# Performance work log

Measured on AMD Instinct MI355X. Metric: run time of the kernel, lower is better.

Reference implementation:

```python
import jax, jax.numpy as jnp
import numpy as np

B, S, D = 4, 2048, 1024
NH, NKV = 16, 4
HD = D // NH  # 64


def _rope(x, freqs):
    # x: [B, H, S, HD], freqs: [B, S, HD//2]
    cos = jnp.concatenate([jnp.cos(freqs), jnp.cos(freqs)], axis=-1)[:, None]  # [B,1,S,HD]
    sin = jnp.concatenate([jnp.sin(freqs), jnp.sin(freqs)], axis=-1)[:, None]
    x1, x2 = x[..., : HD // 2], x[..., HD // 2:]
    rot = jnp.concatenate([-x2, x1], axis=-1)
    return x * cos + rot * sin


def setup_inputs() -> dict:
    key = jax.random.key(0)
    ks = jax.random.split(key, 9)
    return {
        "hidden_states": jax.random.normal(ks[0], (B, S, D), jnp.float32),
        "rotary_pos_emb": jax.random.normal(ks[1], (B, S, HD // 2), jnp.float32),
        "Wq": jax.random.normal(ks[2], (D, NH * HD), jnp.float32) * 0.02,
        "bq": jax.random.normal(ks[3], (NH * HD,), jnp.float32) * 0.02,
        "Wk": jax.random.normal(ks[4], (D, NKV * HD), jnp.float32) * 0.02,
        "bk": jax.random.normal(ks[5], (NKV * HD,), jnp.float32) * 0.02,
        "Wv": jax.random.normal(ks[6], (D, NKV * HD), jnp.float32) * 0.02,
        "bv": jax.random.normal(ks[7], (NKV * HD,), jnp.float32) * 0.02,
        "Wo": jax.random.normal(ks[8], (NH * HD, D), jnp.float32) * 0.02,
    }


def reference(hidden_states, rotary_pos_emb, Wq, bq, Wk, bk, Wv, bv, Wo):
    b, s, _ = hidden_states.shape
    # projections -> [B, H, S, HD]
    q = (hidden_states @ Wq + bq).reshape(b, s, NH, HD).transpose(0, 2, 1, 3)
    k = (hidden_states @ Wk + bk).reshape(b, s, NKV, HD).transpose(0, 2, 1, 3)
    v = (hidden_states @ Wv + bv).reshape(b, s, NKV, HD).transpose(0, 2, 1, 3)
    q = _rope(q, rotary_pos_emb)
    k = _rope(k, rotary_pos_emb)
    groups = NH // NKV
    k = jnp.repeat(k, groups, axis=1)  # [B, NH, S, HD]
    v = jnp.repeat(v, groups, axis=1)
    scaling = HD ** -0.5
    scores = jnp.einsum("bhqd,bhkd->bhqk", q, k) * scaling
    probs = jax.nn.softmax(scores.astype(jnp.float32), axis=-1).astype(q.dtype)
    out = jnp.einsum("bhqk,bhkd->bhqd", probs, v)
    out = out.transpose(0, 2, 1, 3).reshape(b, s, NH * HD)
    return out @ Wo
```

## Files before the change

### kernel.cpp

```cpp
#include <hip/hip_runtime.h>
#include <hip/hip_bf16.h>

#define BB 4
#define SS 2048
#define DD 1024
#define NH 16
#define NKV 4
#define HD 64
#define MROWS (BB*SS)
#define NQKV (NH*HD + 2*NKV*HD)
#define KOFF (NH*HD)

typedef short v8s __attribute__((ext_vector_type(8)));
typedef short v4s __attribute__((ext_vector_type(4)));
typedef float v4f __attribute__((ext_vector_type(4)));
typedef unsigned short u16;
typedef unsigned int u32;

__device__ __forceinline__ float bf2f(u16 u){
  union { float f; u32 i; } x; x.i = ((u32)u) << 16; return x.f;
}
__device__ __forceinline__ u16 f2bf(float f){
  union { __hip_bfloat16 h; u16 u; } x; x.h = __float2bfloat16(f); return x.u;
}
__device__ __forceinline__ u32 cvtpk(float lo, float hi){
  u32 r;
  asm("v_cvt_pk_bf16_f32 %0, %1, %2" : "=v"(r) : "v"(lo), "v"(hi));
  return r;
}
__device__ __forceinline__ void gl_lds16(const u16* g, u16* l){
  __builtin_amdgcn_global_load_lds(
      (const __attribute__((address_space(1))) u32*)g,
      (__attribute__((address_space(3))) u32*)l, 16, 0, 0);
}


__global__ void prep_fused(const float* __restrict__ Wq, const float* __restrict__ Wk,
                           const float* __restrict__ Wv, const float* __restrict__ bq,
                           const float* __restrict__ bk, const float* __restrict__ bv,
                           const float* __restrict__ Wo, const float* __restrict__ fr,
                           u16* __restrict__ Bqkv, float* __restrict__ bias,
                           u16* __restrict__ WoT, float2* __restrict__ trig){
  __shared__ float T[32][33];
  const int bid = blockIdx.x;
  const int tid = threadIdx.x;
  const int tx = tid & 31, ty = tid >> 5;
  if (bid < 1536) {
    const int kt = (bid & 31)*32, nt = (bid >> 5)*32;
    const int n = nt + tx;
    const float* src; int ld, nb;
    if (nt < 1024)      { src = Wq; ld = 1024; nb = n; }
    else if (nt < 1280) { src = Wk; ld = 256;  nb = n - 1024; }
    else                { src = Wv; ld = 256;  nb = n - 1280; }
    #pragma unroll
    for (int i=0;i<4;i++)
      T[ty + 8*i][tx] = src[(long)(kt + ty + 8*i)*ld + nb];
    __syncthreads();
    #pragma unroll
    for (int i=0;i<4;i++)
      Bqkv[(long)(nt + ty + 8*i)*1024 + kt + tx] = f2bf(T[tx][ty + 8*i]);
    if ((bid & 31) == 0 && ty == 0)
      bias[n] = (n < 1024) ? bq[n] : (n < 1280 ? bk[n-1024] : bv[n-1280]);
  } else if (bid < 2560) {
    const int b2 = bid - 1536;
    const int kt = (b2 & 31)*32, nt = (b2 >> 5)*32;
    #pragma unroll
    for (int i=0;i<4;i++)
      T[ty + 8*i][tx] = Wo[(long)(kt + ty + 8*i)*1024 + nt + tx];
    __syncthreads();
    #pragma unroll
    for (int i=0;i<4;i++)
      WoT[(long)(nt + ty + 8*i)*1024 + kt + tx] = f2bf(T[tx][ty + 8*i]);
  } else {
    int i = (bid - 2560)*256 + tid;
    float f = fr[i];
    float sn, cs; __sincosf(f, &sn, &cs);
    trig[i] = make_float2(cs, sn);
  }
}

__global__ void rope_k(u16* __restrict__ QKV, const float2* __restrict__ trig){
  int idx = blockIdx.x*256 + threadIdx.x;
  int d  = idx & 31;
  int hh = (idx >> 5) & 3;
  long row = idx >> 7;
  int col = KOFF + hh*HD + d;
  u16* p = QKV + row*NQKV;
  float x1 = bf2f(p[col]);
  float x2 = bf2f(p[col+32]);
  float2 t = trig[row*32 + d];
  p[col]    = f2bf(x1*t.x - x2*t.y);
  p[col+32] = f2bf(x2*t.x + x1*t.y);
}


template<bool BIAS, typename IT, typename OT>
__global__ __launch_bounds__(256) void gemm_bt(
    const IT* __restrict__ A, const u16* __restrict__ Bt,
    const float* __restrict__ bias, OT* __restrict__ C,
    int K, int ldc)
{
  __shared__ u16 As[128*32];
  __shared__ u16 Bs[128*32];
  const int tid = threadIdx.x;
  const int wid = tid >> 6, lane = tid & 63;
  const int g = lane >> 4, c = lane & 15;
  const long brow = (long)blockIdx.y * 128;
  const long bcol = (long)blockIdx.x * 128;
  const int wr = (wid >> 1) * 64, wc = (wid & 1) * 64;
  const int srow = tid >> 2;
  const int scol = (tid & 3) * 8;
  const IT*  ga = &A [(brow + srow)*K + scol];
  const u16* gb = &Bt[(bcol + srow)*K + scol];
  u16* la  = &As[(wid*64)*8];
  u16* lb  = &Bs[(wid*64)*8];
  u16* lwa = &As[srow*32 + scol];
  v4f acc[4][4] = {};
  for (int kt = 0; kt < K; kt += 32) {
    __syncthreads();
    gl_lds16(gb + kt,        lb);
    gl_lds16(gb + 64*K + kt, lb + 256*8);
    if constexpr (sizeof(IT) == 4) {
      float4 a0 = *reinterpret_cast<const float4*>(ga + kt);
      float4 a1 = *reinterpret_cast<const float4*>(ga + kt + 4);
      float4 a2 = *reinterpret_cast<const float4*>(ga + (long)64*K + kt);
      float4 a3 = *reinterpret_cast<const float4*>(ga + (long)64*K + kt + 4);
      union { v8s v; u32 w[4]; } p0, p1;
      p0.w[0] = cvtpk(a0.x, a0.y); p0.w[1] = cvtpk(a0.z, a0.w);
      p0.w[2] = cvtpk(a1.x, a1.y); p0.w[3] = cvtpk(a1.z, a1.w);
      p1.w[0] = cvtpk(a2.x, a2.y); p1.w[1] = cvtpk(a2.z, a2.w);
      p1.w[2] = cvtpk(a3.x, a3.y); p1.w[3] = cvtpk(a3.z, a3.w);
      *reinterpret_cast<v8s*>(lwa)          = p0.v;
      *reinterpret_cast<v8s*>(lwa + 64*32)  = p1.v;
    } else {
      gl_lds16((const u16*)ga + kt,        la);
      gl_lds16((const u16*)ga + 64*K + kt, la + 256*8);
    }
    __syncthreads();
    v8s af[4], bf[4];
    #pragma unroll
    for (int m=0;m<4;m++) af[m] = *reinterpret_cast<const v8s*>(&As[(wr + m*16 + c)*32 + g*8]);
    #pragma unroll
    for (int n=0;n<4;n++) bf[n] = *reinterpret_cast<const v8s*>(&Bs[(wc + n*16 + c)*32 + g*8]);
    __builtin_amdgcn_s_setprio(1);
    #pragma unroll
    for (int m=0;m<4;m++)
      #pragma unroll
      for (int n=0;n<4;n++)
        acc[m][n] = __builtin_amdgcn_mfma_f32_16x16x32_bf16(af[m], bf[n], acc[m][n], 0,0,0);
    __builtin_amdgcn_s_setprio(0);
  }
  #pragma unroll
  for (int m=0;m<4;m++)
    #pragma unroll
    for (int n=0;n<4;n++) {
      int col = (int)bcol + wc + n*16 + c;
      float badd = BIAS ? bias[col] : 0.0f;
      #pragma unroll
      for (int r2=0;r2<4;r2++){
        long row = brow + wr + m*16 + g*4 + r2;
        float v = acc[m][n][r2] + badd;
        if constexpr (sizeof(OT)==2) C[row*ldc + col] = (OT)f2bf(v);
        else                         C[row*ldc + col] = (OT)v;
      }
    }
}


__global__ __launch_bounds__(512) void attn_k(const u16* __restrict__ QKV,
                                              const float2* __restrict__ trig,
                                              u16* __restrict__ Out){
  __shared__ u16 Ks[4][64][72];
  __shared__ u16 Vs[4][64][72];
  const int tid = threadIdx.x;
  const int wid = tid >> 6, lane = tid & 63;
  const int g = lane >> 4, c = lane & 15;
  const int qt = blockIdx.x & 7;
  const int bh = blockIdx.x >> 3;
  const int b = bh >> 4, h = bh & 15;
  const int kvh = h >> 2;
  const u16* Qb = QKV + (long)b*SS*NQKV + h*HD;
  const u16* Kb = QKV + (long)b*SS*NQKV + KOFF + kvh*HD;
  const u16* Vb = Kb + NKV*HD;

  const float SCL = 0.125f * 1.44269504088896f;
  v8s qf[2][2];
  #pragma unroll
  for (int qn=0;qn<2;qn++){
    int lrow = qt*256 + wid*32 + qn*16 + c;
    v8s q0 = *reinterpret_cast<const v8s*>(&Qb[(long)lrow*NQKV + g*8]);
    v8s q1 = *reinterpret_cast<const v8s*>(&Qb[(long)lrow*NQKV + 32 + g*8]);
    const float2* tp = trig + ((long)b*SS + lrow)*32 + g*8;
    union { v8s v; u32 w[4]; } a0, a1;
    #pragma unroll
    for (int wi=0;wi<4;wi++){
      float2 ta = tp[2*wi], tb = tp[2*wi+1];
      float x1a = bf2f((u16)q0[2*wi]),   x2a = bf2f((u16)q1[2*wi]);
      float x1b = bf2f((u16)q0[2*wi+1]), x2b = bf2f((u16)q1[2*wi+1]);
      float r0a = (x1a*ta.x - x2a*ta.y) * SCL;
      float r1a = (x2a*ta.x + x1a*ta.y) * SCL;
      float r0b = (x1b*tb.x - x2b*tb.y) * SCL;
      float r1b = (x2b*tb.x + x1b*tb.y) * SCL;
      a0.w[wi] = cvtpk(r0a, r0b);
      a1.w[wi] = cvtpk(r1a, r1b);
    }
    qf[qn][0] = a0.v; qf[qn][1] = a1.v;
  }

  v8s onesf;
  {
    short ov = (c==0) ? (short)0x3F80 : (short)0;
    #pragma unroll
    for (int j=0;j<8;j++) onesf[j] = ov;
  }

  const v4f vzero = {0.f, 0.f, 0.f, 0.f};
  v4f o[2][5] = {};

  const int krow = tid >> 3;
  const int kcol = (tid & 7) * 8;
  const int key0 = 2*(tid >> 4);
  const int dg4  = (tid & 15) * 4;
  const int slot0 = 32*(key0>>5) + 8*((key0>>2)&3) + 4*((key0>>4)&1) + (key0&3);
  int vofs[4];
  #pragma unroll
  for (int j=0;j<4;j++){
    int d = dg4 + j;
    int idx = (((slot0>>3) ^ (d>>3)) << 3) | (slot0 & 7);
    vofs[j] = d*72 + idx;
  }
  u16* VsF = &Vs[0][0][0];

  const u16* kp  = Kb + (long)krow*NQKV + kcol;
  const u16* vp0 = Vb + (long)key0*NQKV + dg4;
  const u16* vp1 = vp0 + NQKV;

  v8s kregA, kregB;
  union { v4s v; u32 w[2]; } vrA0, vrA1, vrB0, vrB1;

  auto write_tile = [&](int q, const v8s& kr,
                        const u32* wA, const u32* wB){
    *reinterpret_cast<v8s*>(&Ks[q][krow][kcol]) = kr;
    const int bofs = q * (64*72);
    #pragma unroll
    for (int j=0;j<4;j++){
      u32 pkd = __builtin_amdgcn_perm(wB[j>>1], wA[j>>1],
                                      (j&1) ? 0x07060302u : 0x05040100u);
      *reinterpret_cast<u32*>(&VsF[bofs + vofs[j]]) = pkd;
    }
  };

  auto qk_tile = [&](int buf, v4f st[4][2]){
    v8s kf0[4], kf1[4];
    #pragma unroll
    for (int km=0;km<4;km++){
      kf0[km] = *reinterpret_cast<const v8s*>(&Ks[buf][km*16 + c][g*8]);
      kf1[km] = *reinterpret_cast<const v8s*>(&Ks[buf][km*16 + c][32 + g*8]);
    }
    __builtin_amdgcn_s_setprio(1);
    #pragma unroll
    for (int km=0;km<4;km++)
      #pragma unroll
      for (int qn=0;qn<2;qn++)
        st[km][qn] = __builtin_amdgcn_mfma_f32_16x16x32_bf16(kf0[km], qf[qn][0], vzero, 0,0,0);
    #pragma unroll
    for (int km=0;km<4;km++)
      #pragma unroll
      for (int qn=0;qn<2;qn++)
        st[km][qn] = __builtin_amdgcn_mfma_f32_16x16x32_bf16(kf1[km], qf[qn][1], st[km][qn], 0,0,0);
    __builtin_amdgcn_s_setprio(0);
  };
  auto exp_pack = [&](v4f st[4][2], v8s pa[2][2]){
    #pragma unroll
    for (int km=0;km<4;km++)
      #pragma unroll
      for (int qn=0;qn<2;qn++)
        #pragma unroll
        for (int r2=0;r2<4;r2++)
          st[km][qn][r2] = __builtin_amdgcn_exp2f(st[km][qn][r2]);
    #pragma unroll
    for (int qm=0;qm<2;qm++)
      #pragma unroll
      for (int ks=0;ks<2;ks++){
        union { v8s v; u32 w[4]; } u;
        u.w[0] = cvtpk(st[2*ks  ][qm][0], st[2*ks  ][qm][1]);
        u.w[1] = cvtpk(st[2*ks  ][qm][2], st[2*ks  ][qm][3]);
        u.w[2] = cvtpk(st[2*ks+1][qm][0], st[2*ks+1][qm][1]);
        u.w[3] = cvtpk(st[2*ks+1][qm][2], st[2*ks+1][qm][3]);
        pa[qm][ks] = u.v;
      }
  };
  auto pv_tile = [&](int buf, v8s pa[2][2]){
    #pragma unroll
    for (int ks=0;ks<2;ks++){
      __builtin_amdgcn_s_setprio(1);
      #pragma unroll
      for (int dn=0;dn<4;dn++){
        int d0 = dn*16 + c;
        v8s vf = *reinterpret_cast<const v8s*>(&Vs[buf][d0][(((ks*4+g) ^ (d0>>3)) << 3)]);
        #pragma unroll
        for (int qm=0;qm<2;qm++)
          o[qm][dn] = __builtin_amdgcn_mfma_f32_16x16x32_bf16(pa[qm][ks], vf, o[qm][dn], 0,0,0);
      }
      #pragma unroll
      for (int qm=0;qm<2;qm++)
        o[qm][4] = __builtin_amdgcn_mfma_f32_16x16x32_bf16(pa[qm][ks], onesf, o[qm][4], 0,0,0);
      __builtin_amdgcn_s_setprio(0);
    }
  };

  {
    long off1 = (long)64*NQKV;
    kregA  = *reinterpret_cast<const v8s*>(kp);
    vrA0.v = *reinterpret_cast<const v4s*>(vp0);
    vrA1.v = *reinterpret_cast<const v4s*>(vp1);
    kregB  = *reinterpret_cast<const v8s*>(kp  + off1);
    vrB0.v = *reinterpret_cast<const v4s*>(vp0 + off1);
    vrB1.v = *reinterpret_cast<const v4s*>(vp1 + off1);
    write_tile(0, kregA, vrA0.w, vrA1.w);
    write_tile(1, kregB, vrB0.w, vrB1.w);
  }
  __syncthreads();

  for (int j = 0; j < SS/128; ++j){
    const int base = (j & 1) * 2;
    const bool pf = (j + 1 < SS/128);
    if (pf) {
      long offA = (long)(2*j+2)*64*NQKV;
      long offB = (long)(2*j+3)*64*NQKV;
      kregA  = *reinterpret_cast<const v8s*>(kp  + offA);
      vrA0.v = *reinterpret_cast<const v4s*>(vp0 + offA);
      vrA1.v = *reinterpret_cast<const v4s*>(vp1 + offA);
      kregB  = *reinterpret_cast<const v8s*>(kp  + offB);
      vrB0.v = *reinterpret_cast<const v4s*>(vp0 + offB);
      vrB1.v = *reinterpret_cast<const v4s*>(vp1 + offB);
    }

    v4f stA[4][2];
    v8s paA[2][2], paB[2][2];
    qk_tile(base, stA);
    exp_pack(stA, paA);
    {
      v4f stB[4][2];
      qk_tile(base + 1, stB);
      if (pf) write_tile(base ^ 2, kregA, vrA0.w, vrA1.w);
      pv_tile(base, paA);
      exp_pack(stB, paB);
    }
    if (pf) write_tile((base ^ 2) + 1, kregB, vrB0.w, vrB1.w);
    pv_tile(base + 1, paB);

    __syncthreads();
  }

  #pragma unroll
  for (int qm=0;qm<2;qm++)
    #pragma unroll
    for (int r2=0;r2<4;r2++){
      float l = __shfl(o[qm][4][r2], lane & 48);
      float inv = 1.0f / l;
      long row = (long)b*SS + qt*256 + wid*32 + qm*16 + g*4 + r2;
      #pragma unroll
      for (int dn=0;dn<4;dn++)
        Out[row*DD + h*HD + dn*16 + c] = f2bf(o[qm][dn][r2] * inv);
    }
}


extern "C" void kernel_launch(void* const* d_in, const int* in_sizes, int n_in,
                              void* d_out, int out_size, void* d_ws, size_t ws_size,
                              hipStream_t stream)
{
  const float* hs = (const float*)d_in[0];
  const float* fr = (const float*)d_in[1];
  const float* Wq = (const float*)d_in[2];
  const float* bq = (const float*)d_in[3];
  const float* Wk = (const float*)d_in[4];
  const float* bk = (const float*)d_in[5];
  const float* Wv = (const float*)d_in[6];
  const float* bv = (const float*)d_in[7];
  const float* Wo = (const float*)d_in[8];
  float* out = (float*)d_out;
  char* ws = (char*)d_ws;

  float2* trig = (float2*)ws;
  u16*   Bqkv = (u16*)(ws + 16777216);
  u16*   WoT  = (u16*)(ws + 16777216 + 3145728);
  float* bias = (float*)(ws + 16777216 + 3145728 + 2097152);
  u16*   QKV  = (u16*)(ws + 22028288);
  u16*   AO   = (u16*)(ws + 22028288 + 25165824);

  prep_fused<<<3584, 256, 0, stream>>>(Wq, Wk, Wv, bq, bk, bv, Wo, fr,
                                       Bqkv, bias, WoT, trig);
  gemm_bt<true,  float, u16> <<<dim3(NQKV/128, MROWS/128), 256, 0, stream>>>(hs, Bqkv, bias, QKV, DD, NQKV);
  rope_k    <<<MROWS*NKV*32/256, 256, 0, stream>>>(QKV, trig);
  attn_k    <<<BB*NH*(SS/256), 512, 0, stream>>>(QKV, trig, AO);
  gemm_bt<false, u16, float><<<dim3(DD/128, MROWS/128), 256, 0, stream>>>(AO, WoT, nullptr, out, DD, DD);
}
```

Baseline: 161.6 us.

## Double-buffer LDS tiles in gemm_bt to overlap loads with MFMA

The GEMM kernel now keeps two LDS buffers for the A and B tiles. It issues the next k-tile's global-to-LDS loads before computing on the current tile, leaving one barrier per iteration instead of two. The aim is to hide global load latency behind the MFMA work. LDS use doubles to 32KB per block, which may lower occupancy. The fp32 A path still does synchronous register loads and converts before the MFMAs, so only part of that latency overlaps.

```diff
diff --git a/kernel.cpp b/kernel.cpp
--- a/kernel.cpp
+++ b/kernel.cpp
@@ -100,8 +100,8 @@
     const float* __restrict__ bias, OT* __restrict__ C,
     int K, int ldc)
 {
-  __shared__ u16 As[128*32];
-  __shared__ u16 Bs[128*32];
+  __shared__ u16 As[2][128*32];
+  __shared__ u16 Bs[2][128*32];
   const int tid = threadIdx.x;
   const int wid = tid >> 6, lane = tid & 63;
   const int g = lane >> 4, c = lane & 15;
@@ -112,14 +112,11 @@
   const int scol = (tid & 3) * 8;
   const IT*  ga = &A [(brow + srow)*K + scol];
   const u16* gb = &Bt[(bcol + srow)*K + scol];
-  u16* la  = &As[(wid*64)*8];
-  u16* lb  = &Bs[(wid*64)*8];
-  u16* lwa = &As[srow*32 + scol];
-  v4f acc[4][4] = {};
-  for (int kt = 0; kt < K; kt += 32) {
-    __syncthreads();
-    gl_lds16(gb + kt,        lb);
-    gl_lds16(gb + 64*K + kt, lb + 256*8);
+  const int ldst = (wid*64)*8;
+
+  auto stage = [&](int p, int kt){
+    gl_lds16(gb + kt,        &Bs[p][ldst]);
+    gl_lds16(gb + 64*K + kt, &Bs[p][ldst + 256*8]);
     if constexpr (sizeof(IT) == 4) {
       float4 a0 = *reinterpret_cast<const float4*>(ga + kt);
       float4 a1 = *reinterpret_cast<const float4*>(ga + kt + 4);
@@ -130,18 +127,25 @@
       p0.w[2] = cvtpk(a1.x, a1.y); p0.w[3] = cvtpk(a1.z, a1.w);
       p1.w[0] = cvtpk(a2.x, a2.y); p1.w[1] = cvtpk(a2.z, a2.w);
       p1.w[2] = cvtpk(a3.x, a3.y); p1.w[3] = cvtpk(a3.z, a3.w);
-      *reinterpret_cast<v8s*>(lwa)          = p0.v;
-      *reinterpret_cast<v8s*>(lwa + 64*32)  = p1.v;
+      *reinterpret_cast<v8s*>(&As[p][srow*32 + scol])         = p0.v;
+      *reinterpret_cast<v8s*>(&As[p][srow*32 + scol + 64*32]) = p1.v;
     } else {
-      gl_lds16((const u16*)ga + kt,        la);
-      gl_lds16((const u16*)ga + 64*K + kt, la + 256*8);
-    }
-    __syncthreads();
+      gl_lds16((const u16*)ga + kt,        &As[p][ldst]);
+      gl_lds16((const u16*)ga + 64*K + kt, &As[p][ldst + 256*8]);
+    }
+  };
+
+  v4f acc[4][4] = {};
+  stage(0, 0);
+  __syncthreads();
+  int cur = 0;
+  for (int kt = 0; kt < K; kt += 32) {
+    if (kt + 32 < K) stage(cur ^ 1, kt + 32);
     v8s af[4], bf[4];
     #pragma unroll
-    for (int m=0;m<4;m++) af[m] = *reinterpret_cast<const v8s*>(&As[(wr + m*16 + c)*32 + g*8]);
-    #pragma unroll
-    for (int n=0;n<4;n++) bf[n] = *reinterpret_cast<const v8s*>(&Bs[(wc + n*16 + c)*32 + g*8]);
+    for (int m=0;m<4;m++) af[m] = *reinterpret_cast<const v8s*>(&As[cur][(wr + m*16 + c)*32 + g*8]);
+    #pragma unroll
+    for (int n=0;n<4;n++) bf[n] = *reinterpret_cast<const v8s*>(&Bs[cur][(wc + n*16 + c)*32 + g*8]);
     __builtin_amdgcn_s_setprio(1);
     #pragma unroll
     for (int m=0;m<4;m++)
@@ -149,6 +153,8 @@
       for (int n=0;n<4;n++)
         acc[m][n] = __builtin_amdgcn_mfma_f32_16x16x32_bf16(af[m], bf[n], acc[m][n], 0,0,0);
     __builtin_amdgcn_s_setprio(0);
+    __syncthreads();
+    cur ^= 1;
   }
   #pragma unroll
   for (int m=0;m<4;m++)
```

Result: slower. 166.1 us (+2.8%).
